# Optimization experiments

Hardware: AMD Instinct MI355X
Metric: run time of the kernel (lower is better)

Reference implementation:

```python
import jax, jax.numpy as jnp
import numpy as np
import math

D_MODEL = 1024
N_HEADS = 16
HEAD_DIM = D_MODEL // N_HEADS
PAD_INDEX = 0
NEG_INF = -1e9  # matches torch masked_fill value


def setup_inputs() -> dict:
    key = jax.random.key(0)
    ks = jax.random.split(key, 10)
    b, s = 2, 2048
    x = jax.random.normal(ks[0], (b, s, D_MODEL), dtype=jnp.float32)
    input_ids = jax.random.randint(ks[1], (b, s), 0, 32000, dtype=jnp.int64)
    scale = 1.0 / math.sqrt(D_MODEL)
    def lin(k):
        kw, kb = jax.random.split(k)
        W = jax.random.uniform(kw, (D_MODEL, D_MODEL), jnp.float32, -scale, scale)
        bb = jax.random.uniform(kb, (D_MODEL,), jnp.float32, -scale, scale)
        return W, bb
    Wq, bq = lin(ks[2])
    Wk, bk = lin(ks[3])
    Wv, bv = lin(ks[4])
    Wo, bo = lin(ks[5])
    return {"x": x, "input_ids": input_ids,
            "Wq": Wq, "bq": bq, "Wk": Wk, "bk": bk,
            "Wv": Wv, "bv": bv, "Wo": Wo, "bo": bo}


def reference(x, input_ids, Wq, bq, Wk, bk, Wv, bv, Wo, bo):
    b, s, _ = x.shape
    # torch nn.Linear: y = x @ W.T + b
    q = (x @ Wq.T + bq).reshape(b, s, N_HEADS, HEAD_DIM)
    k = (x @ Wk.T + bk).reshape(b, s, N_HEADS, HEAD_DIM)
    v = (x @ Wv.T + bv).reshape(b, s, N_HEADS, HEAD_DIM)
    # scores: [b, h, s, s]
    scores = jnp.einsum('bqhd,bkhd->bhqk', q, k) / math.sqrt(HEAD_DIM)
    pad_mask = (input_ids != PAD_INDEX)[:, None, None, :]          # [b,1,1,s] over keys
    causal = jnp.tril(jnp.ones((s, s), dtype=bool))[None, None]     # [1,1,s,s]
    final_mask = pad_mask & causal
    scores = jnp.where(final_mask, scores, NEG_INF)
    attn = jax.nn.softmax(scores, axis=-1)
    out = jnp.einsum('bhqk,bkhd->bqhd', attn, v).reshape(b, s, D_MODEL)
    return out @ Wo.T + bo
```

## Files before the change

kernel.cpp:

```cpp
#include <hip/hip_runtime.h>

#define DMODEL 1024
#define NHEADS 16
#define HDIM   64
#define BATCH  2
#define SEQ    2048
#define MROWS  (BATCH*SEQ)

typedef __bf16 bf16x8 __attribute__((ext_vector_type(8)));
typedef __bf16 bf16x4 __attribute__((ext_vector_type(4)));
typedef float floatx4 __attribute__((ext_vector_type(4)));

typedef const __attribute__((address_space(1))) void gvoid;
typedef __attribute__((address_space(3))) void lvoid;

template<bool V> struct ICb { static constexpr bool value = V; };

#define QSCALE 0.18033688011112042f

__global__ void cast_all(const float* __restrict__ x,
                         const float* __restrict__ wq, const float* __restrict__ wk,
                         const float* __restrict__ wv, const float* __restrict__ wo,
                         __bf16* __restrict__ xb, __bf16* __restrict__ wqb,
                         __bf16* __restrict__ wkb, __bf16* __restrict__ wvb,
                         __bf16* __restrict__ wob)
{
  const int i = blockIdx.x * 256 + threadIdx.x;
  const float* s; __bf16* o; int off;
  if (i < MROWS*DMODEL/4) { s = x; o = xb; off = i; }
  else {
    const int r = i - MROWS*DMODEL/4;
    const int w = r >> 18;
    off = r & 262143;
    s = (w == 0) ? wq : (w == 1) ? wk : (w == 2) ? wv : wo;
    o = (w == 0) ? wqb : (w == 1) ? wkb : (w == 2) ? wvb : wob;
  }
  const float4 f = ((const float4*)s)[off];
  bf16x4 v = {(__bf16)f.x, (__bf16)f.y, (__bf16)f.z, (__bf16)f.w};
  *(bf16x4*)(o + off*4) = v;
}

template<int MODE>
__global__ __launch_bounds__(256, 3)
void gemm_nt(const unsigned short* __restrict__ A,
             const unsigned short* __restrict__ W0,
             const unsigned short* __restrict__ W1,
             const unsigned short* __restrict__ W2,
             const float* __restrict__ b0,
             const float* __restrict__ b1,
             const float* __restrict__ b2,
             unsigned short* __restrict__ qout,
             unsigned short* __restrict__ kout,
             unsigned short* __restrict__ vout,
             float* __restrict__ outf)
{
  const int K = DMODEL;
  __shared__ unsigned short As[2][128*32];
  __shared__ unsigned short Bs[2][128*32];
  const int tid  = threadIdx.x;
  const int wid  = tid >> 6;
  const int lane = tid & 63;

  const int lin = blockIdx.x;
  const int wg  = (MODE == 0) ? ((lin & 7)*96 + (lin >> 3))
                              : ((lin & 7)*32 + (lin >> 3));
  const int bx  = (MODE == 0) ? (wg % 24) : (wg & 7);
  const int by  = (MODE == 0) ? (wg / 24) : (wg >> 3);
  const int brow = by * 128;
  const int bcol = bx * 128;
  const int wr = (wid >> 1) * 64;
  const int wc = (wid & 1) * 64;

  int which = 0;
  const unsigned short* Bw = W0;
  const float* bias = b0;
  int bcolL = bcol;
  if (MODE == 0) {
    which = bcol >> 10;
    Bw   = which == 0 ? W0 : which == 1 ? W1 : W2;
    bias = which == 0 ? b0 : which == 1 ? b1 : b2;
    bcolL = bcol & 1023;
  }

  floatx4 acc[4][4] = {};

  const int sr = wid*16 + (lane >> 2);
  const int sc = (lane & 3) * 8;
  const int fr = lane & 15;
  const int fk = (lane >> 4) * 8;

#define GSTAGE(KT, B) do {                                                     \
    _Pragma("unroll")                                                          \
    for (int i_ = 0; i_ < 2; ++i_) {                                           \
      __builtin_amdgcn_global_load_lds(                                        \
          (gvoid*)(A + (size_t)(brow + i_*64 + sr)*K + (KT) + sc),             \
          (lvoid*)(As[B] + i_*2048 + wid*512), 16, 0, 0);                      \
      __builtin_amdgcn_global_load_lds(                                        \
          (gvoid*)(Bw + (size_t)(bcolL + i_*64 + sr)*K + (KT) + sc),           \
          (lvoid*)(Bs[B] + i_*2048 + wid*512), 16, 0, 0);                      \
    }                                                                          \
  } while (0)

  GSTAGE(0, 0);

  for (int kt = 0; kt < K; kt += 32) {
    const int cur = (kt >> 5) & 1;
    if (kt + 32 < K) {
      GSTAGE(kt + 32, cur ^ 1);
      asm volatile("s_waitcnt vmcnt(4)" ::: "memory");
    } else {
      asm volatile("s_waitcnt vmcnt(0)" ::: "memory");
    }
    __builtin_amdgcn_s_barrier();
    __builtin_amdgcn_sched_barrier(0);

    bf16x8 af[4], bfv[4];
#pragma unroll
    for (int m = 0; m < 4; ++m)
      af[m] = *(const bf16x8*)(As[cur] + (wr + m*16 + fr)*32 + fk);
#pragma unroll
    for (int n = 0; n < 4; ++n)
      bfv[n] = *(const bf16x8*)(Bs[cur] + (wc + n*16 + fr)*32 + fk);
    __builtin_amdgcn_s_setprio(1);
#pragma unroll
    for (int m = 0; m < 4; ++m)
#pragma unroll
      for (int n = 0; n < 4; ++n)
        acc[m][n] = __builtin_amdgcn_mfma_f32_16x16x32_bf16(af[m], bfv[n], acc[m][n], 0, 0, 0);
    __builtin_amdgcn_s_setprio(0);
    __builtin_amdgcn_s_barrier();
  }
#undef GSTAGE

  const int er = (lane >> 4) * 4;
  const int ec = lane & 15;
#pragma unroll
  for (int m = 0; m < 4; ++m) {
#pragma unroll
    for (int n = 0; n < 4; ++n) {
      const int colL = bcolL + wc + n*16 + ec;
      const float bv = bias[colL];
      const int rowb = brow + wr + m*16 + er;
      if (MODE == 0) {
        const int bi = rowb >> 11, s = rowb & 2047;
        const int hh = colL >> 6, dd = colL & 63;
        if (which == 2) {
          bf16x4 v4 = {(__bf16)(acc[m][n][0] + bv), (__bf16)(acc[m][n][1] + bv),
                       (__bf16)(acc[m][n][2] + bv), (__bf16)(acc[m][n][3] + bv)};
          *(bf16x4*)((__bf16*)vout + ((size_t)(bi*NHEADS + hh)*HDIM + dd)*SEQ + s) = v4;
        } else if (which == 0) {
          __bf16* o = (__bf16*)qout;
#pragma unroll
          for (int j = 0; j < 4; ++j)
            o[((size_t)(bi*NHEADS + hh)*SEQ + s + j)*HDIM + dd] =
                (__bf16)((acc[m][n][j] + bv) * QSCALE);
        } else {
          __bf16* o = (__bf16*)kout;
#pragma unroll
          for (int j = 0; j < 4; ++j)
            o[((size_t)(bi*NHEADS + hh)*SEQ + s + j)*HDIM + dd] = (__bf16)(acc[m][n][j] + bv);
        }
      } else {
#pragma unroll
        for (int j = 0; j < 4; ++j)
          outf[(size_t)(rowb + j)*DMODEL + colL] = acc[m][n][j] + bv;
      }
    }
  }
}

__global__ __launch_bounds__(512, 4)
void attn_fwd(const unsigned short* __restrict__ qb,
              const unsigned short* __restrict__ kb,
              const unsigned short* __restrict__ vtb,
              const int* __restrict__ ids,
              unsigned short* __restrict__ outb)
{
  const int hb = blockIdx.x;
  const int pr = blockIdx.y;
  const int h = hb & 15, bi = hb >> 4;

  const int tid = threadIdx.x, wid = tid >> 6, lane = tid & 63;
  const int grp  = wid >> 2;
  const int wid4 = wid & 3;
  const size_t hoff = (size_t)(bi*NHEADS + h) * SEQ * HDIM;
  const unsigned short* Qh  = qb  + hoff;
  const unsigned short* Kh  = kb  + hoff;
  const unsigned short* Vth = vtb + hoff;

  __shared__ unsigned short Ks[2][2][64*64];
  __shared__ unsigned short Vs[2][2][64*64];
  __shared__ unsigned short Ps[8][16*64];
  float* LOf = (float*)Ps;
  float* Ll  = (float*)Ks;

  const int q_   = lane & 15;
  const int hi4  = lane >> 4;
  const int koff = hi4 * 4;

  const int gt = tid & 255;
  const int r0 = gt >> 3;
  const int sw = ((gt & 7) ^ (r0 & 7)) * 8;
  unsigned short* Pw = Ps[wid];

#define STAGE(T, B) do {                                                       \
    const unsigned short* kbase_ = Kh + (size_t)((T)*64) * HDIM;               \
    const unsigned short* vbase_ = Vth + (T)*64;                               \
    __builtin_amdgcn_global_load_lds((gvoid*)(kbase_ + r0*64 + sw),            \
                                     (lvoid*)(Ks[grp][B] + gt*8), 16, 0, 0);   \
    __builtin_amdgcn_global_load_lds((gvoid*)(kbase_ + (r0+32)*64 + sw),       \
                                     (lvoid*)(Ks[grp][B] + (gt+256)*8), 16, 0, 0);\
    __builtin_amdgcn_global_load_lds((gvoid*)(vbase_ + (size_t)r0*SEQ + sw),   \
                                     (lvoid*)(Vs[grp][B] + gt*8), 16, 0, 0);   \
    __builtin_amdgcn_global_load_lds((gvoid*)(vbase_ + (size_t)(r0+32)*SEQ + sw),\
                                     (lvoid*)(Vs[grp][B] + (gt+256)*8), 16, 0, 0);\
  } while (0)

  for (int half = 0; half < 2; ++half) {
    const int qt = half ? 31 - pr : pr;
    const int qbase = qt * 64;
    const int qg = qbase + wid4*16 + q_;

    bf16x8 qf[2];
#pragma unroll
    for (int c = 0; c < 2; ++c)
      qf[c] = *(const bf16x8*)(Qh + (size_t)qg*HDIM + c*32 + hi4*8);

    float lsum = 0.f;
    floatx4 Oacc[4] = {};

    auto step = [&](auto Mc, int kb0, int bufc, unsigned long long wm) {
      constexpr bool MASKED = decltype(Mc)::value;

      floatx4 st[4];
      __builtin_amdgcn_s_setprio(1);
#pragma unroll
      for (int t = 0; t < 4; ++t) {
        st[t] = (floatx4){0.f, 0.f, 0.f, 0.f};
        const int kr = t*16 + q_;
#pragma unroll
        for (int c = 0; c < 2; ++c) {
          const int cd = ((c*4 + hi4) ^ (kr & 7)) * 8;
          bf16x8 kf = *(const bf16x8*)(Ks[grp][bufc] + kr*64 + cd);
          st[t] = __builtin_amdgcn_mfma_f32_16x16x32_bf16(kf, qf[c], st[t], 0, 0, 0);
        }
      }
      __builtin_amdgcn_s_setprio(0);

      float ps = 0.f;
#pragma unroll
      for (int t = 0; t < 4; ++t) {
        float p[4];
#pragma unroll
        for (int r = 0; r < 4; ++r) {
          float pv = exp2f(st[t][r]);
          if (MASKED) {
            const int ko = t*16 + koff + r;
            const bool dead = ((kb0 + ko) > qg) || (((wm >> ko) & 1ull) != 0ull);
            pv = dead ? 0.f : pv;
          }
          p[r] = pv;
          ps += pv;
        }
        bf16x4 pk = {(__bf16)p[0], (__bf16)p[1], (__bf16)p[2], (__bf16)p[3]};
        const int ko = t*16 + koff;
        *(bf16x4*)(Pw + q_*64 + (((ko >> 3) ^ (q_ & 7)) * 8) + (ko & 7)) = pk;
      }
      lsum += ps;

      __builtin_amdgcn_s_setprio(1);
#pragma unroll
      for (int cp = 0; cp < 2; ++cp) {
        const int ko = cp*32 + hi4*8;
        bf16x8 pf = *(const bf16x8*)(Pw + q_*64 + (((ko >> 3) ^ (q_ & 7)) * 8));
#pragma unroll
        for (int n = 0; n < 4; ++n) {
          const int d = n*16 + q_;
          const int cd = ((cp*4 + hi4) ^ (d & 7)) * 8;
          bf16x8 vf = *(const bf16x8*)(Vs[grp][bufc] + d*64 + cd);
          Oacc[n] = __builtin_amdgcn_mfma_f32_16x16x32_bf16(pf, vf, Oacc[n], 0, 0, 0);
        }
      }
      __builtin_amdgcn_s_setprio(0);
    };

    const int nT = qt + 1;
    const int h0 = (nT + 1) >> 1;
    const int cnt = (grp == 0) ? h0 : nT - h0;
    const int tb  = (grp == 0) ? 0 : h0;

    if (cnt > 0) STAGE(tb, 0);

    for (int i = 0; i < h0; ++i) {
      const bool valid = (i < cnt);
      const int t = tb + i;
      const int kb0 = t * 64;
      int pv = 1;
      if (valid) pv = ids[bi*SEQ + kb0 + lane];
      if (i + 1 < cnt) {
        STAGE(t + 1, (i + 1) & 1);
        asm volatile("s_waitcnt vmcnt(4)" ::: "memory");
      } else {
        asm volatile("s_waitcnt vmcnt(0)" ::: "memory");
      }
      const unsigned long long wm = __ballot(pv == 0);
      __builtin_amdgcn_s_barrier();
      __builtin_amdgcn_sched_barrier(0);

      if (valid) {
        const int bufc = i & 1;
        if ((t != nT - 1) && wm == 0ull) step(ICb<false>{}, kb0, bufc, 0ull);
        else                             step(ICb<true >{}, kb0, bufc, wm);
      }
      __builtin_amdgcn_s_barrier();
    }

    float lt = lsum + __shfl_xor(lsum, 16);
    lt += __shfl_xor(lt, 32);

    if (grp == 1) {
#pragma unroll
      for (int r = 0; r < 4; ++r)
#pragma unroll
        for (int n = 0; n < 4; ++n)
          LOf[(wid4*16 + koff + r)*64 + n*16 + q_] = Oacc[n][r];
      if (hi4 == 0) Ll[wid4*16 + q_] = lt;
    }
    __syncthreads();
    if (grp == 0) {
#pragma unroll
      for (int r = 0; r < 4; ++r) {
        const int rloc = wid4*16 + koff + r;
        const float inv = 1.f / (__shfl(lt, koff + r) + Ll[rloc]);
        const int row = bi*SEQ + qbase + rloc;
#pragma unroll
        for (int n = 0; n < 4; ++n) {
          const float o = Oacc[n][r] + LOf[rloc*64 + n*16 + q_];
          ((__bf16*)outb)[(size_t)row*DMODEL + h*HDIM + n*16 + q_] = (__bf16)(o * inv);
        }
      }
    }
    __syncthreads();
  }
#undef STAGE
}

extern "C" void kernel_launch(void* const* d_in, const int* in_sizes, int n_in,
                              void* d_out, int out_size, void* d_ws, size_t ws_size,
                              hipStream_t stream)
{
  const float* x  = (const float*)d_in[0];
  const int*   ids= (const int*)d_in[1];
  const float* Wq = (const float*)d_in[2];
  const float* bq = (const float*)d_in[3];
  const float* Wk = (const float*)d_in[4];
  const float* bk = (const float*)d_in[5];
  const float* Wv = (const float*)d_in[6];
  const float* bv = (const float*)d_in[7];
  const float* Wo = (const float*)d_in[8];
  const float* bo = (const float*)d_in[9];
  float* out = (float*)d_out;

  char* ws = (char*)d_ws;
  unsigned short* xb   = (unsigned short*)(ws);
  unsigned short* wqb  = (unsigned short*)(ws + ( 8u<<20));
  unsigned short* wkb  = (unsigned short*)(ws + (10u<<20));
  unsigned short* wvb  = (unsigned short*)(ws + (12u<<20));
  unsigned short* wob  = (unsigned short*)(ws + (14u<<20));
  unsigned short* qbuf = (unsigned short*)(ws + (16u<<20));
  unsigned short* kbuf = (unsigned short*)(ws + (24u<<20));
  unsigned short* vbuf = (unsigned short*)(ws + (32u<<20));
  unsigned short* abuf = (unsigned short*)(ws + (40u<<20));

  cast_all<<<8192, 256, 0, stream>>>(x, Wq, Wk, Wv, Wo,
                                     (__bf16*)xb, (__bf16*)wqb, (__bf16*)wkb,
                                     (__bf16*)wvb, (__bf16*)wob);

  gemm_nt<0><<<768, 256, 0, stream>>>(xb, wqb, wkb, wvb, bq, bk, bv,
                                      qbuf, kbuf, vbuf, nullptr);

  attn_fwd<<<dim3(32, 16), 512, 0, stream>>>(qbuf, kbuf, vbuf, ids, abuf);

  gemm_nt<1><<<256, 256, 0, stream>>>(abuf, wob, wob, wob, bo, bo, bo,
                                      nullptr, nullptr, nullptr, out);
}
```

Measured before the change: 111.7 us.

## Add dedicated output-projection GEMM with 128x64 tiles, BK=64, swizzled LDS; widen cast

Splits the templated GEMM into a QKV GEMM and a separate output-projection kernel. The new kernel uses 128x64 tiles with a K-step of 64 and an XOR-swizzled LDS layout, and launches 512 workgroups instead of 256. The goal is better CU occupancy on the smaller output GEMM and fewer LDS bank conflicts. The cast kernel now handles 8 elements per thread with 16-byte stores, halving its grid, which trades fewer loop iterations for some extra register pressure.

```diff
diff --git a/kernel.cpp b/kernel.cpp
--- a/kernel.cpp
+++ b/kernel.cpp
@@ -25,34 +25,34 @@
                          __bf16* __restrict__ wkb, __bf16* __restrict__ wvb,
                          __bf16* __restrict__ wob)
 {
-  const int i = blockIdx.x * 256 + threadIdx.x;
+  const int u = blockIdx.x * 256 + threadIdx.x;
   const float* s; __bf16* o; int off;
-  if (i < MROWS*DMODEL/4) { s = x; o = xb; off = i; }
+  if (u < MROWS*DMODEL/8) { s = x; o = xb; off = u; }
   else {
-    const int r = i - MROWS*DMODEL/4;
-    const int w = r >> 18;
-    off = r & 262143;
+    const int r = u - MROWS*DMODEL/8;
+    const int w = r >> 17;
+    off = r & 131071;
     s = (w == 0) ? wq : (w == 1) ? wk : (w == 2) ? wv : wo;
     o = (w == 0) ? wqb : (w == 1) ? wkb : (w == 2) ? wvb : wob;
   }
-  const float4 f = ((const float4*)s)[off];
-  bf16x4 v = {(__bf16)f.x, (__bf16)f.y, (__bf16)f.z, (__bf16)f.w};
-  *(bf16x4*)(o + off*4) = v;
+  const float4 f0 = ((const float4*)s)[off*2];
+  const float4 f1 = ((const float4*)s)[off*2 + 1];
+  bf16x8 v = {(__bf16)f0.x, (__bf16)f0.y, (__bf16)f0.z, (__bf16)f0.w,
+              (__bf16)f1.x, (__bf16)f1.y, (__bf16)f1.z, (__bf16)f1.w};
+  *(bf16x8*)(o + off*8) = v;
 }
 
-template<int MODE>
 __global__ __launch_bounds__(256, 3)
-void gemm_nt(const unsigned short* __restrict__ A,
-             const unsigned short* __restrict__ W0,
-             const unsigned short* __restrict__ W1,
-             const unsigned short* __restrict__ W2,
-             const float* __restrict__ b0,
-             const float* __restrict__ b1,
-             const float* __restrict__ b2,
-             unsigned short* __restrict__ qout,
-             unsigned short* __restrict__ kout,
-             unsigned short* __restrict__ vout,
-             float* __restrict__ outf)
+void gemm_qkv(const unsigned short* __restrict__ A,
+              const unsigned short* __restrict__ W0,
+              const unsigned short* __restrict__ W1,
+              const unsigned short* __restrict__ W2,
+              const float* __restrict__ b0,
+              const float* __restrict__ b1,
+              const float* __restrict__ b2,
+              unsigned short* __restrict__ qout,
+              unsigned short* __restrict__ kout,
+              unsigned short* __restrict__ vout)
 {
   const int K = DMODEL;
   __shared__ unsigned short As[2][128*32];
@@ -62,25 +62,18 @@
   const int lane = tid & 63;
 
   const int lin = blockIdx.x;
-  const int wg  = (MODE == 0) ? ((lin & 7)*96 + (lin >> 3))
-                              : ((lin & 7)*32 + (lin >> 3));
-  const int bx  = (MODE == 0) ? (wg % 24) : (wg & 7);
-  const int by  = (MODE == 0) ? (wg / 24) : (wg >> 3);
+  const int wg  = (lin & 7)*96 + (lin >> 3);
+  const int bx  = wg % 24;
+  const int by  = wg / 24;
   const int brow = by * 128;
   const int bcol = bx * 128;
   const int wr = (wid >> 1) * 64;
   const int wc = (wid & 1) * 64;
 
-  int which = 0;
-  const unsigned short* Bw = W0;
-  const float* bias = b0;
-  int bcolL = bcol;
-  if (MODE == 0) {
-    which = bcol >> 10;
-    Bw   = which == 0 ? W0 : which == 1 ? W1 : W2;
-    bias = which == 0 ? b0 : which == 1 ? b1 : b2;
-    bcolL = bcol & 1023;
-  }
+  const int which = bcol >> 10;
+  const unsigned short* Bw = which == 0 ? W0 : which == 1 ? W1 : W2;
+  const float* bias = which == 0 ? b0 : which == 1 ? b1 : b2;
+  const int bcolL = bcol & 1023;
 
   floatx4 acc[4][4] = {};
 
@@ -141,30 +134,123 @@
       const int colL = bcolL + wc + n*16 + ec;
       const float bv = bias[colL];
       const int rowb = brow + wr + m*16 + er;
-      if (MODE == 0) {
-        const int bi = rowb >> 11, s = rowb & 2047;
-        const int hh = colL >> 6, dd = colL & 63;
-        if (which == 2) {
-          bf16x4 v4 = {(__bf16)(acc[m][n][0] + bv), (__bf16)(acc[m][n][1] + bv),
-                       (__bf16)(acc[m][n][2] + bv), (__bf16)(acc[m][n][3] + bv)};
-          *(bf16x4*)((__bf16*)vout + ((size_t)(bi*NHEADS + hh)*HDIM + dd)*SEQ + s) = v4;
-        } else if (which == 0) {
-          __bf16* o = (__bf16*)qout;
-#pragma unroll
-          for (int j = 0; j < 4; ++j)
-            o[((size_t)(bi*NHEADS + hh)*SEQ + s + j)*HDIM + dd] =
-                (__bf16)((acc[m][n][j] + bv) * QSCALE);
-        } else {
-          __bf16* o = (__bf16*)kout;
-#pragma unroll
-          for (int j = 0; j < 4; ++j)
-            o[((size_t)(bi*NHEADS + hh)*SEQ + s + j)*HDIM + dd] = (__bf16)(acc[m][n][j] + bv);
-        }
+      const int bi = rowb >> 11, s = rowb & 2047;
+      const int hh = colL >> 6, dd = colL & 63;
+      if (which == 2) {
+        bf16x4 v4 = {(__bf16)(acc[m][n][0] + bv), (__bf16)(acc[m][n][1] + bv),
+                     (__bf16)(acc[m][n][2] + bv), (__bf16)(acc[m][n][3] + bv)};
+        *(bf16x4*)((__bf16*)vout + ((size_t)(bi*NHEADS + hh)*HDIM + dd)*SEQ + s) = v4;
+      } else if (which == 0) {
+        __bf16* o = (__bf16*)qout;
+#pragma unroll
+        for (int j = 0; j < 4; ++j)
+          o[((size_t)(bi*NHEADS + hh)*SEQ + s + j)*HDIM + dd] =
+              (__bf16)((acc[m][n][j] + bv) * QSCALE);
       } else {
+        __bf16* o = (__bf16*)kout;
 #pragma unroll
         for (int j = 0; j < 4; ++j)
-          outf[(size_t)(rowb + j)*DMODEL + colL] = acc[m][n][j] + bv;
-      }
+          o[((size_t)(bi*NHEADS + hh)*SEQ + s + j)*HDIM + dd] = (__bf16)(acc[m][n][j] + bv);
+      }
+    }
+  }
+}
+
+__global__ __launch_bounds__(256, 3)
+void gemm_out(const unsigned short* __restrict__ A,
+              const unsigned short* __restrict__ W,
+              const float* __restrict__ bias,
+              float* __restrict__ outf)
+{
+  const int K = DMODEL;
+  __shared__ unsigned short As[2][128*64];
+  __shared__ unsigned short Bs[2][64*64];
+  const int tid  = threadIdx.x;
+  const int wid  = tid >> 6;
+  const int lane = tid & 63;
+
+  const int lin = blockIdx.x;
+  const int wg  = (lin & 7)*64 + (lin >> 3);
+  const int bx  = wg & 15;
+  const int by  = wg >> 4;
+  const int brow = by * 128;
+  const int bcol = bx * 64;
+  const int wr = (wid >> 1) * 64;
+  const int wc = (wid & 1) * 32;
+
+  floatx4 acc[4][2] = {};
+
+  const int fr  = lane & 15;
+  const int hi4 = lane >> 4;
+
+  const int r0 = tid >> 3;
+  const int sw = ((tid & 7) ^ (r0 & 7)) * 8;
+
+  auto gstage = [&](int kt, int B) {
+#pragma unroll
+    for (int i_ = 0; i_ < 4; ++i_)
+      __builtin_amdgcn_global_load_lds(
+          (gvoid*)(A + (size_t)(brow + i_*32 + r0)*K + kt + sw),
+          (lvoid*)(As[B] + (i_*256 + tid)*8), 16, 0, 0);
+#pragma unroll
+    for (int i_ = 0; i_ < 2; ++i_)
+      __builtin_amdgcn_global_load_lds(
+          (gvoid*)(W + (size_t)(bcol + i_*32 + r0)*K + kt + sw),
+          (lvoid*)(Bs[B] + (i_*256 + tid)*8), 16, 0, 0);
+  };
+
+  gstage(0, 0);
+
+  for (int kt = 0; kt < K; kt += 64) {
+    const int cur = (kt >> 6) & 1;
+    if (kt + 64 < K) {
+      gstage(kt + 64, cur ^ 1);
+      asm volatile("s_waitcnt vmcnt(6)" ::: "memory");
+    } else {
+      asm volatile("s_waitcnt vmcnt(0)" ::: "memory");
+    }
+    __builtin_amdgcn_s_barrier();
+    __builtin_amdgcn_sched_barrier(0);
+
+    bf16x8 af[4][2], bfv[2][2];
+#pragma unroll
+    for (int m = 0; m < 4; ++m) {
+      const int ra = wr + m*16 + fr;
+#pragma unroll
+      for (int c = 0; c < 2; ++c)
+        af[m][c] = *(const bf16x8*)(As[cur] + ra*64 + (((c*4 + hi4) ^ (ra & 7)) * 8));
+    }
+#pragma unroll
+    for (int n = 0; n < 2; ++n) {
+      const int rb = wc + n*16 + fr;
+#pragma unroll
+      for (int c = 0; c < 2; ++c)
+        bfv[n][c] = *(const bf16x8*)(Bs[cur] + rb*64 + (((c*4 + hi4) ^ (rb & 7)) * 8));
+    }
+    __builtin_amdgcn_s_setprio(1);
+#pragma unroll
+    for (int m = 0; m < 4; ++m)
+#pragma unroll
+      for (int n = 0; n < 2; ++n)
+#pragma unroll
+        for (int c = 0; c < 2; ++c)
+          acc[m][n] = __builtin_amdgcn_mfma_f32_16x16x32_bf16(af[m][c], bfv[n][c], acc[m][n], 0, 0, 0);
+    __builtin_amdgcn_s_setprio(0);
+    __builtin_amdgcn_s_barrier();
+  }
+
+  const int er = hi4 * 4;
+  const int ec = lane & 15;
+#pragma unroll
+  for (int m = 0; m < 4; ++m) {
+#pragma unroll
+    for (int n = 0; n < 2; ++n) {
+      const int col = bcol + wc + n*16 + ec;
+      const float bv = bias[col];
+      const int rowb = brow + wr + m*16 + er;
+#pragma unroll
+      for (int j = 0; j < 4; ++j)
+        outf[(size_t)(rowb + j)*DMODEL + col] = acc[m][n][j] + bv;
     }
   }
 }
@@ -372,15 +458,14 @@
   unsigned short* vbuf = (unsigned short*)(ws + (32u<<20));
   unsigned short* abuf = (unsigned short*)(ws + (40u<<20));
 
-  cast_all<<<8192, 256, 0, stream>>>(x, Wq, Wk, Wv, Wo,
+  cast_all<<<4096, 256, 0, stream>>>(x, Wq, Wk, Wv, Wo,
                                      (__bf16*)xb, (__bf16*)wqb, (__bf16*)wkb,
                                      (__bf16*)wvb, (__bf16*)wob);
 
-  gemm_nt<0><<<768, 256, 0, stream>>>(xb, wqb, wkb, wvb, bq, bk, bv,
-                                      qbuf, kbuf, vbuf, nullptr);
+  gemm_qkv<<<768, 256, 0, stream>>>(xb, wqb, wkb, wvb, bq, bk, bv,
+                                    qbuf, kbuf, vbuf);
 
   attn_fwd<<<dim3(32, 16), 512, 0, stream>>>(qbuf, kbuf, vbuf, ids, abuf);
 
-  gemm_nt<1><<<256, 256, 0, stream>>>(abuf, wob, wob, wob, bo, bo, bo,
-                                      nullptr, nullptr, nullptr, out);
+  gemm_out<<<512, 256, 0, stream>>>(abuf, wob, bo, out);
 }
```

After: 105.4 us (median of 3 runs). -5.7%, faster.
